# Optimization experiments

Measured on AMD Instinct MI355X. Metric: run time of the kernel, lower is better.

The kernel has to match this reference:

```python
import jax, jax.numpy as jnp
import numpy as np


def setup_inputs() -> dict:
    key = jax.random.key(0)
    ks = jax.random.split(key, 5)
    B, C, D, H, W = 2, 256, 8, 28, 28
    mid = C // 2
    # Kaiming-normal-ish init (std = sqrt(2/fan_in)) for 1x1 conv weights
    def kaiming(k, shape, fan_in):
        return jax.random.normal(k, shape, dtype=jnp.float32) * np.sqrt(2.0 / fan_in)
    x = jax.random.normal(ks[0], (B, C, D, H, W), dtype=jnp.float32)
    w1 = kaiming(ks[1], (mid, C), C)
    w2 = kaiming(ks[2], (mid, C), C)
    w3 = kaiming(ks[3], (mid, C), C)
    w4 = kaiming(ks[4], (C, mid), mid)
    b1 = jnp.zeros((mid,), jnp.float32)
    b2 = jnp.zeros((mid,), jnp.float32)
    b3 = jnp.zeros((mid,), jnp.float32)
    b4 = jnp.zeros((C,), jnp.float32)
    return {"x": x, "w1": w1, "b1": b1, "w2": w2, "b2": b2,
            "w3": w3, "b3": b3, "w4": w4, "b4": b4}


def reference(x, w1, b1, w2, b2, w3, b3, w4, b4):
    # x: [B, C, D, H, W]; 1x1x1 Conv3d == channel matmul over flattened N = D*H*W
    B, C, D, H, W = x.shape
    N = D * H * W
    xf = x.reshape(B, C, N)                                   # [B, C, N]
    # theta: conv1 -> [B, N, mid]
    e1 = jnp.einsum('mc,bcn->bnm', w1, xf) + b1               # [B, N, mid]
    # phi: conv2 -> [B, mid, N]
    e2 = jnp.einsum('mc,bcn->bmn', w2, xf) + b2[:, None]      # [B, mid, N]
    # g: conv3 -> [B, N, mid]
    e3 = jnp.einsum('mc,bcn->bnm', w3, xf) + b3               # [B, N, mid]
    # unscaled attention: softmax over keys (last axis)
    kernel = jnp.einsum('bnm,bmk->bnk', e1, e2)               # [B, N, N]
    kernel = jax.nn.softmax(kernel, axis=2)
    attn = jnp.einsum('bnk,bkm->bnm', kernel, e3)             # [B, N, mid]
    # conv4 (1x1 Conv1d): mid -> C, applied on [B, mid, N]
    y = jnp.einsum('cm,bnm->bcn', w4, attn) + b4[:, None]     # [B, C, N]
    return x + y.reshape(B, C, D, H, W)
```

## Files before the change

kernel.cpp:

```cpp
#include <hip/hip_runtime.h>


#define BB  2
#define CC  256
#define NN  6272
#define MID 128
#define KS  4
#define QB  128
#define NT  (NN / 64)
#define LOG2E 1.4426950408889634f

typedef _Float16 half2_t __attribute__((ext_vector_type(2)));
typedef _Float16 half4_t __attribute__((ext_vector_type(4)));
typedef _Float16 half8_t __attribute__((ext_vector_type(8)));
typedef float    floatx16 __attribute__((ext_vector_type(16)));
typedef int      i32x2 __attribute__((ext_vector_type(2)));
typedef unsigned u32x4 __attribute__((ext_vector_type(4)));

__device__ __forceinline__ unsigned pkrtz(float a, float b) {
    return __builtin_bit_cast(unsigned, __builtin_amdgcn_cvt_pkrtz(a, b));
}
__device__ __forceinline__ half8_t cvt8(const float* p) {
    float4 f0 = *(const float4*)p;
    float4 f1 = *(const float4*)(p + 4);
    u32x4 u;
    u[0] = pkrtz(f0.x, f0.y); u[1] = pkrtz(f0.z, f0.w);
    u[2] = pkrtz(f1.x, f1.y); u[3] = pkrtz(f1.z, f1.w);
    return __builtin_bit_cast(half8_t, u);
}

__global__ __launch_bounds__(256, 2) void proj_kernel(
    const float* __restrict__ x,
    const float* __restrict__ w1, const float* __restrict__ bi1,
    const float* __restrict__ w2, const float* __restrict__ bi2,
    const float* __restrict__ w3, const float* __restrict__ bi3,
    _Float16* __restrict__ Qg, _Float16* __restrict__ Kg, _Float16* __restrict__ VtG)
{
    const int t    = threadIdx.x;
    const int lane = t & 63;
    const int wave = t >> 6;
    const int l31  = lane & 31;
    const int l5   = lane >> 5;
    const int n0   = blockIdx.x * 32;
    const int b    = blockIdx.y;

    __shared__ _Float16 xhi[32 * 260];
    __shared__ _Float16 xlo[32 * 260];

    #pragma unroll
    for (int a = t; a < 512; a += 256) {
        int cg = a >> 3, ng = a & 7;
        int c  = cg * 4, n4 = ng * 4;
        const float* xb = x + ((size_t)b * CC + c) * NN + n0 + n4;
        float4 v0 = *(const float4*)(xb);
        float4 v1 = *(const float4*)(xb + NN);
        float4 v2 = *(const float4*)(xb + 2 * (size_t)NN);
        float4 v3 = *(const float4*)(xb + 3 * (size_t)NN);
        const float* pv[4] = {&v0.x, &v1.x, &v2.x, &v3.x};
        #pragma unroll
        for (int nn = 0; nn < 4; ++nn) {
            half4_t h, l;
            #pragma unroll
            for (int ci = 0; ci < 4; ++ci) {
                float f = pv[ci][nn];
                _Float16 hh = (_Float16)f;
                h[ci] = hh;
                l[ci] = (_Float16)(f - (float)hh);
            }
            *(half4_t*)&xhi[(n4 + nn) * 260 + c] = h;
            *(half4_t*)&xlo[(n4 + nn) * 260 + c] = l;
        }
    }
    __syncthreads();

    floatx16 acc[3];
    #pragma unroll
    for (int i = 0; i < 3; ++i)
        #pragma unroll
        for (int j = 0; j < 16; ++j) acc[i][j] = 0.f;

    #pragma unroll
    for (int i = 0; i < 3; ++i) {
        const int tau = wave * 3 + i;
        const int pj = tau >> 2, mt = tau & 3;
        const float* w = (pj == 0) ? w1 : (pj == 1) ? w2 : w3;
        const float* wrow = w + (size_t)(mt * 32 + l31) * CC + l5 * 8;
        const _Float16* xr_hi = xhi + l31 * 260 + l5 * 8;
        const _Float16* xr_lo = xlo + l31 * 260 + l5 * 8;
        #pragma unroll
        for (int ds = 0; ds < 16; ++ds) {
            half8_t wf = cvt8(wrow + ds * 16);
            half8_t ah = *(const half8_t*)(xr_hi + ds * 16);
            half8_t al = *(const half8_t*)(xr_lo + ds * 16);
            if (pj < 2) {
                acc[i] = __builtin_amdgcn_mfma_f32_32x32x16_f16(ah, wf, acc[i], 0, 0, 0);
                acc[i] = __builtin_amdgcn_mfma_f32_32x32x16_f16(al, wf, acc[i], 0, 0, 0);
            } else {
                acc[i] = __builtin_amdgcn_mfma_f32_32x32x16_f16(wf, ah, acc[i], 0, 0, 0);
                acc[i] = __builtin_amdgcn_mfma_f32_32x32x16_f16(wf, al, acc[i], 0, 0, 0);
            }
        }
    }

    #pragma unroll
    for (int i = 0; i < 3; ++i) {
        const int tau = wave * 3 + i;
        const int pj = tau >> 2, mt = tau & 3;
        if (pj < 2) {
            const float bm = ((pj == 0) ? bi1 : bi2)[mt * 32 + l31];
            const float sc = (pj == 0) ? LOG2E : 1.0f;
            _Float16* eo = ((pj == 0) ? Qg : Kg) + (size_t)b * NN * MID;
            #pragma unroll
            for (int j = 0; j < 16; ++j) {
                int n = n0 + (j & 3) + 8 * (j >> 2) + 4 * l5;
                eo[(size_t)n * MID + mt * 32 + l31] = (_Float16)((acc[i][j] + bm) * sc);
            }
        } else {
            _Float16* eo = VtG + (size_t)b * MID * NN;
            #pragma unroll
            for (int j = 0; j < 16; ++j) {
                int m = mt * 32 + (j & 3) + 8 * (j >> 2) + 4 * l5;
                eo[(size_t)m * NN + n0 + l31] = (_Float16)(acc[i][j] + bi3[m]);
            }
        }
    }
}

__global__ __launch_bounds__(256, 2) void attn_kernel(
    const _Float16* __restrict__ Qg, const _Float16* __restrict__ Kg,
    const _Float16* __restrict__ VtG, _Float16* __restrict__ Opart,
    float* __restrict__ MLg)
{
    const int t    = threadIdx.x;
    const int lane = t & 63;
    const int wave = t >> 6;
    const int l31  = lane & 31;
    const int l5   = lane >> 5;
    const int c8   = blockIdx.x & 7;
    const int b    = c8 >> 2;
    const int sp   = c8 & 3;
    const int q0   = (blockIdx.x >> 3) * QB;
    const int kt0  = (NT * sp) / KS;
    const int kt1  = (NT * (sp + 1)) / KS;

    __shared__ __align__(16) char lds[69632];
    _Float16* Ks0 = (_Float16*)lds;
    _Float16* Ks1 = (_Float16*)(lds + 17408);
    _Float16* Vt0 = (_Float16*)(lds + 34816);
    _Float16* Vt1 = (_Float16*)(lds + 52224);
    _Float16* Osh = (_Float16*)lds;

    const _Float16* Qb = Qg + ((size_t)b * NN + q0 + wave * 32) * MID;
    const _Float16* Kb = Kg + (size_t)b * NN * MID;
    const _Float16* Vb = VtG + (size_t)b * MID * NN;

    half8_t qf[8];
    #pragma unroll
    for (int ds = 0; ds < 8; ++ds)
        qf[ds] = *(const half8_t*)(Qb + (size_t)l31 * MID + ds * 16 + l5 * 8);

    floatx16 o[4];
    #pragma unroll
    for (int dt = 0; dt < 4; ++dt)
        #pragma unroll
        for (int j = 0; j < 16; ++j) o[dt][j] = 0.f;
    float m_run = -3.0e38f, l_run = 0.f;

    const int krow_t = t >> 4, koff_t = (t & 15) * 8;
    const int vd_t   = t >> 3, voff_t = (t & 7) * 8;

    #pragma unroll
    for (int it = 0; it < 4; ++it) {
        int r = it * 16 + krow_t;
        *(half8_t*)(Ks0 + r * 136 + koff_t) =
            *(const half8_t*)(Kb + (size_t)(kt0 * 64 + r) * MID + koff_t);
    }
    #pragma unroll
    for (int it = 0; it < 4; ++it) {
        int d = it * 32 + vd_t;
        *(half8_t*)(Vt0 + d * 68 + voff_t) =
            *(const half8_t*)(Vb + (size_t)d * NN + kt0 * 64 + voff_t);
    }
    __syncthreads();

    for (int kt = kt0, cbuf = 0; kt < kt1; ++kt, cbuf ^= 1) {
        const int nk = kt * 64;
        _Float16* KBcur = cbuf ? Ks1 : Ks0;
        _Float16* KBnxt = cbuf ? Ks0 : Ks1;
        _Float16* VBcur = cbuf ? Vt1 : Vt0;
        _Float16* VBnxt = cbuf ? Vt0 : Vt1;

        const int nk2 = (kt + 1 < kt1) ? nk + 64 : nk;
        half8_t vreg[4], kreg[4];
        #pragma unroll
        for (int it = 0; it < 4; ++it)
            vreg[it] = *(const half8_t*)(Vb + (size_t)(it * 32 + vd_t) * NN + nk2 + voff_t);
        #pragma unroll
        for (int it = 0; it < 4; ++it)
            kreg[it] = *(const half8_t*)(Kb + (size_t)(nk2 + it * 16 + krow_t) * MID + koff_t);
        __builtin_amdgcn_sched_barrier(0);

        floatx16 s0, s1;
        #pragma unroll
        for (int j = 0; j < 16; ++j) { s0[j] = 0.f; s1[j] = 0.f; }
        const _Float16* krow0 = KBcur + l31 * 136 + l5 * 8;
        const _Float16* krow1 = KBcur + (32 + l31) * 136 + l5 * 8;
        __builtin_amdgcn_s_setprio(1);
        #pragma unroll
        for (int ds = 0; ds < 8; ++ds) {
            s0 = __builtin_amdgcn_mfma_f32_32x32x16_f16(
                     *(const half8_t*)(krow0 + ds * 16), qf[ds], s0, 0, 0, 0);
            s1 = __builtin_amdgcn_mfma_f32_32x32x16_f16(
                     *(const half8_t*)(krow1 + ds * 16), qf[ds], s1, 0, 0, 0);
        }
        __builtin_amdgcn_s_setprio(0);

        float tmax = fmaxf(s0[0], s1[0]);
        #pragma unroll
        for (int j = 1; j < 16; ++j) tmax = fmaxf(tmax, fmaxf(s0[j], s1[j]));
        tmax = fmaxf(tmax, __shfl_xor(tmax, 32));

        if (!__all(tmax <= m_run)) {
            const float m_new = fmaxf(m_run, tmax);
            const float alpha = exp2f(m_run - m_new);
            m_run = m_new;
            l_run *= alpha;
            #pragma unroll
            for (int dt = 0; dt < 4; ++dt)
                #pragma unroll
                for (int j = 0; j < 16; ++j) o[dt][j] *= alpha;
        }

        float psum = 0.f;
        unsigned u0[8], u1[8];
        #pragma unroll
        for (int g = 0; g < 4; ++g) {
            float p0 = exp2f(s0[4 * g + 0] - m_run);
            float p1 = exp2f(s0[4 * g + 1] - m_run);
            float p2 = exp2f(s0[4 * g + 2] - m_run);
            float p3 = exp2f(s0[4 * g + 3] - m_run);
            psum += (p0 + p1) + (p2 + p3);
            u0[g] = pkrtz(p0, p1);
            u1[g] = pkrtz(p2, p3);
        }
        #pragma unroll
        for (int g = 0; g < 4; ++g) {
            float p0 = exp2f(s1[4 * g + 0] - m_run);
            float p1 = exp2f(s1[4 * g + 1] - m_run);
            float p2 = exp2f(s1[4 * g + 2] - m_run);
            float p3 = exp2f(s1[4 * g + 3] - m_run);
            psum += (p0 + p1) + (p2 + p3);
            u0[4 + g] = pkrtz(p0, p1);
            u1[4 + g] = pkrtz(p2, p3);
        }
        psum += __shfl_xor(psum, 32);
        l_run += psum;

        #pragma unroll
        for (int it = 0; it < 4; ++it)
            *(half8_t*)(VBnxt + (it * 32 + vd_t) * 68 + voff_t) = vreg[it];
        #pragma unroll
        for (int it = 0; it < 4; ++it)
            *(half8_t*)(KBnxt + (it * 16 + krow_t) * 136 + koff_t) = kreg[it];

        __builtin_amdgcn_s_setprio(1);
        #pragma unroll
        for (int ks = 0; ks < 4; ++ks) {
            i32x2 rA = __builtin_amdgcn_permlane32_swap(
                           (int)u0[2 * ks], (int)u0[2 * ks + 1], false, false);
            i32x2 rB = __builtin_amdgcn_permlane32_swap(
                           (int)u1[2 * ks], (int)u1[2 * ks + 1], false, false);
            u32x4 pw;
            pw[0] = (unsigned)rA[0]; pw[1] = (unsigned)rB[0];
            pw[2] = (unsigned)rA[1]; pw[3] = (unsigned)rB[1];
            half8_t pf = __builtin_bit_cast(half8_t, pw);
            const _Float16* vcol = VBcur + ks * 16 + l5 * 8;
            #pragma unroll
            for (int dt = 0; dt < 4; ++dt)
                o[dt] = __builtin_amdgcn_mfma_f32_32x32x16_f16(
                            *(const half8_t*)(vcol + (dt * 32 + l31) * 68), pf,
                            o[dt], 0, 0, 0);
        }
        __builtin_amdgcn_s_setprio(0);

        __syncthreads();
    }

    if (l5 == 0) {
        float* mlb = MLg + ((size_t)(b * KS + sp) * 2) * NN;
        mlb[q0 + wave * 32 + l31]      = m_run;
        mlb[NN + q0 + wave * 32 + l31] = l_run;
    }

    #pragma unroll
    for (int dt = 0; dt < 4; ++dt)
        #pragma unroll
        for (int h = 0; h < 4; ++h) {
            half4_t v;
            #pragma unroll
            for (int i = 0; i < 4; ++i) v[i] = (_Float16)o[dt][4 * h + i];
            *(half4_t*)(Osh + (wave * 32 + l31) * 136 + dt * 32 + 8 * h + 4 * l5) = v;
        }
    __syncthreads();
    _Float16* Ob = Opart + ((size_t)(b * KS + sp) * NN + q0) * MID;
    #pragma unroll
    for (int it = 0; it < 8; ++it) {
        int c = it * 256 + t;
        int q = c >> 4, g = c & 15;
        *(half8_t*)(Ob + (size_t)q * MID + g * 8) =
            *(const half8_t*)(Osh + q * 136 + g * 8);
    }
}

__global__ __launch_bounds__(256, 4) void comb_kernel(
    const _Float16* __restrict__ Opart, const float* __restrict__ MLg,
    _Float16* __restrict__ attnW)
{
    const int t  = threadIdx.x;
    const int b  = blockIdx.y;
    const int q  = blockIdx.x * 32 + (t >> 3);
    const int dg = (t & 7) * 16;

    float mv[KS], lv[KS];
    float m_g = -3.0e38f;
    #pragma unroll
    for (int s = 0; s < KS; ++s) {
        const float* mlb = MLg + ((size_t)(b * KS + s) * 2) * NN;
        mv[s] = mlb[q];
        lv[s] = mlb[NN + q];
        m_g = fmaxf(m_g, mv[s]);
    }
    float lg = 0.f, w[KS];
    #pragma unroll
    for (int s = 0; s < KS; ++s) { w[s] = exp2f(mv[s] - m_g); lg += lv[s] * w[s]; }
    const float inv = 1.0f / lg;

    float acc[16];
    #pragma unroll
    for (int j = 0; j < 16; ++j) acc[j] = 0.f;
    #pragma unroll
    for (int s = 0; s < KS; ++s) {
        const half8_t* Op = (const half8_t*)(Opart + ((size_t)(b * KS + s) * NN + q) * MID + dg);
        half8_t v0 = Op[0], v1 = Op[1];
        #pragma unroll
        for (int j = 0; j < 8; ++j) {
            acc[j]     += (float)v0[j] * w[s];
            acc[8 + j] += (float)v1[j] * w[s];
        }
    }
    half8_t h0, h1;
    #pragma unroll
    for (int j = 0; j < 8; ++j) {
        h0[j] = (_Float16)(acc[j] * inv);
        h1[j] = (_Float16)(acc[8 + j] * inv);
    }
    half8_t* Ow = (half8_t*)(attnW + ((size_t)b * NN + q) * MID + dg);
    Ow[0] = h0; Ow[1] = h1;
}

__global__ __launch_bounds__(256, 2) void epi_kernel(
    const _Float16* __restrict__ attnW, const float* __restrict__ w4,
    const float* __restrict__ b4, const float* __restrict__ x,
    float* __restrict__ out)
{
    const int t    = threadIdx.x;
    const int lane = t & 63;
    const int wave = t >> 6;
    const int l31  = lane & 31;
    const int l5   = lane >> 5;
    const int n0   = blockIdx.x * 32;
    const int b    = blockIdx.y;

    half8_t bf[8];
    const _Float16* brow = attnW + ((size_t)b * NN + n0 + l31) * MID + l5 * 8;
    #pragma unroll
    for (int ds = 0; ds < 8; ++ds)
        bf[ds] = *(const half8_t*)(brow + ds * 16);

    #pragma unroll
    for (int i = 0; i < 2; ++i) {
        const int ct = wave * 2 + i;
        floatx16 acc;
        #pragma unroll
        for (int j = 0; j < 16; ++j) acc[j] = 0.f;

        const float* wrow = w4 + (size_t)(ct * 32 + l31) * MID + l5 * 8;
        #pragma unroll
        for (int ds = 0; ds < 8; ++ds) {
            half8_t wf = cvt8(wrow + ds * 16);
            acc = __builtin_amdgcn_mfma_f32_32x32x16_f16(wf, bf[ds], acc, 0, 0, 0);
        }
        #pragma unroll
        for (int j = 0; j < 16; ++j) {
            int c = ct * 32 + (j & 3) + 8 * (j >> 2) + 4 * l5;
            size_t off = ((size_t)b * CC + c) * NN + n0 + l31;
            out[off] = acc[j] + b4[c] + x[off];
        }
    }
}

extern "C" void kernel_launch(void* const* d_in, const int* in_sizes, int n_in,
                              void* d_out, int out_size, void* d_ws, size_t ws_size,
                              hipStream_t stream)
{
    const float* x  = (const float*)d_in[0];
    const float* w1 = (const float*)d_in[1];
    const float* b1 = (const float*)d_in[2];
    const float* w2 = (const float*)d_in[3];
    const float* b2 = (const float*)d_in[4];
    const float* w3 = (const float*)d_in[5];
    const float* b3 = (const float*)d_in[6];
    const float* w4 = (const float*)d_in[7];
    const float* b4 = (const float*)d_in[8];
    float* out = (float*)d_out;

    _Float16* Qg    = (_Float16*)d_ws;
    _Float16* Kg    = Qg + (size_t)BB * NN * MID;
    _Float16* VtG   = Kg + (size_t)BB * NN * MID;
    _Float16* attnW = VtG + (size_t)BB * NN * MID;
    float* MLg      = (float*)(attnW + (size_t)BB * NN * MID);
    _Float16* Opart = (_Float16*)d_out;

    proj_kernel<<<dim3(NN / 32, BB), 256, 0, stream>>>(x, w1, b1, w2, b2, w3, b3, Qg, Kg, VtG);
    attn_kernel<<<dim3((NN / QB) * KS * BB), 256, 0, stream>>>(Qg, Kg, VtG, Opart, MLg);
    comb_kernel<<<dim3(NN / 32, BB), 256, 0, stream>>>(Opart, MLg, attnW);
    epi_kernel<<<dim3(NN / 32, BB), 256, 0, stream>>>(attnW, w4, b4, x, out);
}
```

Measured before the change: 259.0 us.

## Split each key tile across wave pairs in attention kernel with LDS merge

```diff
diff --git a/kernel.cpp b/kernel.cpp
--- a/kernel.cpp
+++ b/kernel.cpp
@@ -126,7 +126,7 @@
     }
 }
 
-__global__ __launch_bounds__(256, 2) void attn_kernel(
+__global__ __launch_bounds__(512, 4) void attn_kernel(
     const _Float16* __restrict__ Qg, const _Float16* __restrict__ Kg,
     const _Float16* __restrict__ VtG, _Float16* __restrict__ Opart,
     float* __restrict__ MLg)
@@ -134,6 +134,8 @@
     const int t    = threadIdx.x;
     const int lane = t & 63;
     const int wave = t >> 6;
+    const int qs   = wave >> 1;
+    const int kh   = wave & 1;
     const int l31  = lane & 31;
     const int l5   = lane >> 5;
     const int c8   = blockIdx.x & 7;
@@ -143,14 +145,15 @@
     const int kt0  = (NT * sp) / KS;
     const int kt1  = (NT * (sp + 1)) / KS;
 
-    __shared__ __align__(16) char lds[69632];
+    __shared__ __align__(16) char lds[71680];
     _Float16* Ks0 = (_Float16*)lds;
     _Float16* Ks1 = (_Float16*)(lds + 17408);
     _Float16* Vt0 = (_Float16*)(lds + 34816);
     _Float16* Vt1 = (_Float16*)(lds + 52224);
-    _Float16* Osh = (_Float16*)lds;
-
-    const _Float16* Qb = Qg + ((size_t)b * NN + q0 + wave * 32) * MID;
+    float*  stats = (float*)(lds + 69632);
+    float*  Obuf  = (float*)lds;
+
+    const _Float16* Qb = Qg + ((size_t)b * NN + q0 + qs * 32) * MID;
     const _Float16* Kb = Kg + (size_t)b * NN * MID;
     const _Float16* Vb = VtG + (size_t)b * MID * NN;
 
@@ -170,14 +173,14 @@
     const int vd_t   = t >> 3, voff_t = (t & 7) * 8;
 
     #pragma unroll
-    for (int it = 0; it < 4; ++it) {
-        int r = it * 16 + krow_t;
+    for (int it = 0; it < 2; ++it) {
+        int r = it * 32 + krow_t;
         *(half8_t*)(Ks0 + r * 136 + koff_t) =
             *(const half8_t*)(Kb + (size_t)(kt0 * 64 + r) * MID + koff_t);
     }
     #pragma unroll
-    for (int it = 0; it < 4; ++it) {
-        int d = it * 32 + vd_t;
+    for (int it = 0; it < 2; ++it) {
+        int d = it * 64 + vd_t;
         *(half8_t*)(Vt0 + d * 68 + voff_t) =
             *(const half8_t*)(Vb + (size_t)d * NN + kt0 * 64 + voff_t);
     }
@@ -191,33 +194,29 @@
         _Float16* VBnxt = cbuf ? Vt0 : Vt1;
 
         const int nk2 = (kt + 1 < kt1) ? nk + 64 : nk;
-        half8_t vreg[4], kreg[4];
-        #pragma unroll
-        for (int it = 0; it < 4; ++it)
-            vreg[it] = *(const half8_t*)(Vb + (size_t)(it * 32 + vd_t) * NN + nk2 + voff_t);
-        #pragma unroll
-        for (int it = 0; it < 4; ++it)
-            kreg[it] = *(const half8_t*)(Kb + (size_t)(nk2 + it * 16 + krow_t) * MID + koff_t);
+        half8_t vreg[2], kreg[2];
+        #pragma unroll
+        for (int it = 0; it < 2; ++it)
+            vreg[it] = *(const half8_t*)(Vb + (size_t)(it * 64 + vd_t) * NN + nk2 + voff_t);
+        #pragma unroll
+        for (int it = 0; it < 2; ++it)
+            kreg[it] = *(const half8_t*)(Kb + (size_t)(nk2 + it * 32 + krow_t) * MID + koff_t);
         __builtin_amdgcn_sched_barrier(0);
 
-        floatx16 s0, s1;
-        #pragma unroll
-        for (int j = 0; j < 16; ++j) { s0[j] = 0.f; s1[j] = 0.f; }
-        const _Float16* krow0 = KBcur + l31 * 136 + l5 * 8;
-        const _Float16* krow1 = KBcur + (32 + l31) * 136 + l5 * 8;
+        floatx16 s;
+        #pragma unroll
+        for (int j = 0; j < 16; ++j) s[j] = 0.f;
+        const _Float16* krow = KBcur + (kh * 32 + l31) * 136 + l5 * 8;
         __builtin_amdgcn_s_setprio(1);
         #pragma unroll
-        for (int ds = 0; ds < 8; ++ds) {
-            s0 = __builtin_amdgcn_mfma_f32_32x32x16_f16(
-                     *(const half8_t*)(krow0 + ds * 16), qf[ds], s0, 0, 0, 0);
-            s1 = __builtin_amdgcn_mfma_f32_32x32x16_f16(
-                     *(const half8_t*)(krow1 + ds * 16), qf[ds], s1, 0, 0, 0);
-        }
+        for (int ds = 0; ds < 8; ++ds)
+            s = __builtin_amdgcn_mfma_f32_32x32x16_f16(
+                    *(const half8_t*)(krow + ds * 16), qf[ds], s, 0, 0, 0);
         __builtin_amdgcn_s_setprio(0);
 
-        float tmax = fmaxf(s0[0], s1[0]);
-        #pragma unroll
-        for (int j = 1; j < 16; ++j) tmax = fmaxf(tmax, fmaxf(s0[j], s1[j]));
+        float tmax = s[0];
+        #pragma unroll
+        for (int j = 1; j < 16; ++j) tmax = fmaxf(tmax, s[j]);
         tmax = fmaxf(tmax, __shfl_xor(tmax, 32));
 
         if (!__all(tmax <= m_run)) {
@@ -232,40 +231,30 @@
         }
 
         float psum = 0.f;
-        unsigned u0[8], u1[8];
+        unsigned u0[4], u1[4];
         #pragma unroll
         for (int g = 0; g < 4; ++g) {
-            float p0 = exp2f(s0[4 * g + 0] - m_run);
-            float p1 = exp2f(s0[4 * g + 1] - m_run);
-            float p2 = exp2f(s0[4 * g + 2] - m_run);
-            float p3 = exp2f(s0[4 * g + 3] - m_run);
+            float p0 = exp2f(s[4 * g + 0] - m_run);
+            float p1 = exp2f(s[4 * g + 1] - m_run);
+            float p2 = exp2f(s[4 * g + 2] - m_run);
+            float p3 = exp2f(s[4 * g + 3] - m_run);
             psum += (p0 + p1) + (p2 + p3);
             u0[g] = pkrtz(p0, p1);
             u1[g] = pkrtz(p2, p3);
         }
-        #pragma unroll
-        for (int g = 0; g < 4; ++g) {
-            float p0 = exp2f(s1[4 * g + 0] - m_run);
-            float p1 = exp2f(s1[4 * g + 1] - m_run);
-            float p2 = exp2f(s1[4 * g + 2] - m_run);
-            float p3 = exp2f(s1[4 * g + 3] - m_run);
-            psum += (p0 + p1) + (p2 + p3);
-            u0[4 + g] = pkrtz(p0, p1);
-            u1[4 + g] = pkrtz(p2, p3);
-        }
         psum += __shfl_xor(psum, 32);
         l_run += psum;
 
         #pragma unroll
-        for (int it = 0; it < 4; ++it)
-            *(half8_t*)(VBnxt + (it * 32 + vd_t) * 68 + voff_t) = vreg[it];
-        #pragma unroll
-        for (int it = 0; it < 4; ++it)
-            *(half8_t*)(KBnxt + (it * 16 + krow_t) * 136 + koff_t) = kreg[it];
+        for (int it = 0; it < 2; ++it)
+            *(half8_t*)(VBnxt + (it * 64 + vd_t) * 68 + voff_t) = vreg[it];
+        #pragma unroll
+        for (int it = 0; it < 2; ++it)
+            *(half8_t*)(KBnxt + (it * 32 + krow_t) * 136 + koff_t) = kreg[it];
 
         __builtin_amdgcn_s_setprio(1);
         #pragma unroll
-        for (int ks = 0; ks < 4; ++ks) {
+        for (int ks = 0; ks < 2; ++ks) {
             i32x2 rA = __builtin_amdgcn_permlane32_swap(
                            (int)u0[2 * ks], (int)u0[2 * ks + 1], false, false);
             i32x2 rB = __builtin_amdgcn_permlane32_swap(
@@ -274,7 +263,7 @@
             pw[0] = (unsigned)rA[0]; pw[1] = (unsigned)rB[0];
             pw[2] = (unsigned)rA[1]; pw[3] = (unsigned)rB[1];
             half8_t pf = __builtin_bit_cast(half8_t, pw);
-            const _Float16* vcol = VBcur + ks * 16 + l5 * 8;
+            const _Float16* vcol = VBcur + kh * 32 + ks * 16 + l5 * 8;
             #pragma unroll
             for (int dt = 0; dt < 4; ++dt)
                 o[dt] = __builtin_amdgcn_mfma_f32_32x32x16_f16(
@@ -287,28 +276,48 @@
     }
 
     if (l5 == 0) {
+        stats[qs * 64 + kh * 32 + l31]       = m_run;
+        stats[256 + qs * 64 + kh * 32 + l31] = l_run;
+    }
+    __syncthreads();
+    const float m_o  = stats[qs * 64 + (1 ^ kh) * 32 + l31];
+    const float l_o  = stats[256 + qs * 64 + (1 ^ kh) * 32 + l31];
+    const float m_st = fmaxf(m_run, m_o);
+    const float sc   = exp2f(m_run - m_st);
+    const float l_st = l_run * sc + l_o * exp2f(m_o - m_st);
+
+    if (kh == 0 && l5 == 0) {
         float* mlb = MLg + ((size_t)(b * KS + sp) * 2) * NN;
-        mlb[q0 + wave * 32 + l31]      = m_run;
-        mlb[NN + q0 + wave * 32 + l31] = l_run;
-    }
-
-    #pragma unroll
-    for (int dt = 0; dt < 4; ++dt)
-        #pragma unroll
-        for (int h = 0; h < 4; ++h) {
-            half4_t v;
-            #pragma unroll
-            for (int i = 0; i < 4; ++i) v[i] = (_Float16)o[dt][4 * h + i];
-            *(half4_t*)(Osh + (wave * 32 + l31) * 136 + dt * 32 + 8 * h + 4 * l5) = v;
-        }
+        mlb[q0 + qs * 32 + l31]      = m_st;
+        mlb[NN + q0 + qs * 32 + l31] = l_st;
+    }
+
+    if (kh == 1) {
+        #pragma unroll
+        for (int dt = 0; dt < 4; ++dt)
+            #pragma unroll
+            for (int j = 0; j < 16; ++j) {
+                int d = dt * 32 + (j & 3) + 8 * (j >> 2) + 4 * l5;
+                Obuf[(qs * 32 + l31) * 132 + d] = o[dt][j] * sc;
+            }
+    }
+    __syncthreads();
+    if (kh == 0) {
+        #pragma unroll
+        for (int dt = 0; dt < 4; ++dt)
+            #pragma unroll
+            for (int j = 0; j < 16; ++j) {
+                int d = dt * 32 + (j & 3) + 8 * (j >> 2) + 4 * l5;
+                Obuf[(qs * 32 + l31) * 132 + d] += o[dt][j] * sc;
+            }
+    }
     __syncthreads();
     _Float16* Ob = Opart + ((size_t)(b * KS + sp) * NN + q0) * MID;
     #pragma unroll
-    for (int it = 0; it < 8; ++it) {
-        int c = it * 256 + t;
+    for (int it = 0; it < 4; ++it) {
+        int c = it * 512 + t;
         int q = c >> 4, g = c & 15;
-        *(half8_t*)(Ob + (size_t)q * MID + g * 8) =
-            *(const half8_t*)(Osh + q * 136 + g * 8);
+        *(half8_t*)(Ob + (size_t)q * MID + g * 8) = cvt8(Obuf + q * 132 + g * 8);
     }
 }
 
@@ -422,7 +431,7 @@
     _Float16* Opart = (_Float16*)d_out;
 
     proj_kernel<<<dim3(NN / 32, BB), 256, 0, stream>>>(x, w1, b1, w2, b2, w3, b3, Qg, Kg, VtG);
-    attn_kernel<<<dim3((NN / QB) * KS * BB), 256, 0, stream>>>(Qg, Kg, VtG, Opart, MLg);
+    attn_kernel<<<dim3((NN / QB) * KS * BB), 512, 0, stream>>>(Qg, Kg, VtG, Opart, MLg);
     comb_kernel<<<dim3(NN / 32, BB), 256, 0, stream>>>(Opart, MLg, attnW);
     epi_kernel<<<dim3(NN / 32, BB), 256, 0, stream>>>(attnW, w4, b4, x, out);
 }
```

Result: slower. 281.5 us (+8.7%).
